# Performance work log

Hardware: AMD Instinct MI355X
Metric: run time of the kernel (lower is better)

## Reference

```python
import jax, jax.numpy as jnp
import numpy as np

VOCAB, D, S, T, B, E, C = 21128, 768, 50, 5, 512, 128, 10


def gcn(x, edges, W, b):
    # GCNConv with self-loops and symmetric normalization. x: [S, D]
    N = x.shape[0]
    loop = jnp.arange(N)
    src = jnp.concatenate([edges[0], loop])
    dst = jnp.concatenate([edges[1], loop])
    deg = jax.ops.segment_sum(jnp.ones_like(src, dtype=x.dtype), dst, num_segments=N)
    dinv = jax.lax.rsqrt(jnp.maximum(deg, 1e-12))
    norm = dinv[src] * dinv[dst]
    h = x @ W  # [S, 10]
    out = jax.ops.segment_sum(h[src] * norm[:, None], dst, num_segments=N)
    return out + b


def mpm(self_f, cross_f, assign, W1, b1, W2, b2):
    # multi-perspective matching, broadcast over leading dims; node dim = -2
    a = assign * self_f
    c = assign * cross_f
    num = jnp.sum(a * c, axis=-1)
    den = jnp.maximum(jnp.linalg.norm(a, axis=-1) * jnp.linalg.norm(c, axis=-1), 1e-8)
    cos = num / den
    bshape = jnp.broadcast_shapes(self_f.shape[:-2], cross_f.shape[:-2])
    sf = jnp.broadcast_to(self_f, bshape + self_f.shape[-2:])
    h = jnp.concatenate([cos[..., None], sf], axis=-1)  # [..., S, 11]
    h = jax.nn.relu(h @ W1 + b1) @ W2 + b2  # [..., S, 20]
    return jnp.max(h, axis=-2)  # [..., 20]


def setup_inputs() -> dict:
    key = jax.random.key(0)
    ks = jax.random.split(key, 20)
    inp = {
        "context_input": jax.random.randint(ks[0], (B, T, S), 0, VOCAB),
        "response_input": jax.random.randint(ks[1], (B, S), 0, VOCAB),
        "context_graph_adjs": jax.random.randint(ks[2], (B, T, 2, E), 0, S),
        "response_graph_adj": jax.random.randint(ks[3], (B, 2, E), 0, S),
        "word_emb": jax.random.normal(ks[4], (VOCAB, D), jnp.float32) * 0.02,
        "conv_W": jax.random.normal(ks[5], (D, C), jnp.float32) * 0.05,
        "conv_b": jnp.zeros((C,), jnp.float32),
        "cross_w": jax.random.uniform(ks[6], (D, C), jnp.float32),
        "attention_coef": jax.random.uniform(ks[7], (S, S), jnp.float32),
        "assign_weight": jax.random.uniform(ks[8], (S, C), jnp.float32),
        "mp_W1": jax.random.normal(ks[9], (C + 1, 20), jnp.float32) * 0.3,
        "mp_b1": jnp.zeros((20,), jnp.float32),
        "mp_W2": jax.random.normal(ks[10], (20, 20), jnp.float32) * 0.2,
        "mp_b2": jnp.zeros((20,), jnp.float32),
        "ffn_W1": jax.random.normal(ks[11], (80, 40), jnp.float32) * 0.1,
        "ffn_b1": jnp.zeros((40,), jnp.float32),
        "ffn_W2": jax.random.normal(ks[12], (40, 1), jnp.float32) * 0.2,
        "ffn_b2": jnp.zeros((1,), jnp.float32),
    }
    return inp


def reference(context_input, response_input, context_graph_adjs, response_graph_adj,
              word_emb, conv_W, conv_b, cross_w, attention_coef, assign_weight,
              mp_W1, mp_b1, mp_W2, mp_b2, ffn_W1, ffn_b1, ffn_W2, ffn_b2):
    ctx = word_emb[context_input]      # [B, T, S, D]
    resp = word_emb[response_input]    # [B, S, D]

    gcn_b = jax.vmap(gcn, in_axes=(0, 0, None, None))
    resp_gcn = gcn_b(resp, response_graph_adj, conv_W, conv_b)                      # [B, S, C]
    ctx_gcn = jax.vmap(gcn_b, in_axes=(0, 0, None, None))(ctx, context_graph_adjs, conv_W, conv_b)  # [B, T, S, C]

    # cross features: utterance cross comes from response, response cross from utterance
    u_cross = jnp.einsum('ps,bsk->bpk', attention_coef, resp @ cross_w)   # [B, S, C]
    r_cross = jnp.einsum('ps,btsk->btpk', attention_coef, ctx @ cross_w)  # [B, T, S, C]

    g_u = mpm(ctx_gcn, u_cross[:, None], assign_weight, mp_W1, mp_b1, mp_W2, mp_b2)       # [B, T, 20]
    g_r = mpm(resp_gcn[:, None], r_cross, assign_weight, mp_W1, mp_b1, mp_W2, mp_b2)      # [B, T, 20]

    feat = jnp.concatenate([g_u, g_r, g_u * g_r, jnp.abs(g_u - g_r)], axis=-1)  # [B, T, 80]
    logits = jax.nn.relu(feat @ ffn_W1 + ffn_b1) @ ffn_W2 + ffn_b2              # [B, T, 1]
    return jax.nn.sigmoid(jnp.sum(logits, axis=1))                              # [B, 1]
```

## Files before the change

kernel.cpp:

```cpp
#include <hip/hip_runtime.h>
#include <math.h>

#define VOCAB 21128
#define DD 768
#define SS 50
#define TT 5
#define BB 512
#define EE 128
#define CC 10
#define V20 (VOCAB * 20)
#define NG 2560
#define NALL 3072

__global__ __launch_bounds__(512) void k_vocab(const float* __restrict__ emb,
                                               const float* __restrict__ Wconv,
                                               const float* __restrict__ Wcross,
                                               float* __restrict__ hvp) {
    __shared__ float tile[8][64][21];
    const int wv = threadIdx.x >> 6, lane = threadIdx.x & 63;
    const int rowbase = blockIdx.x * 64;
    const int rsub = lane >> 2, m = lane & 3;

    const int d0w = blockIdx.y * 384 + __builtin_amdgcn_readfirstlane(wv * 48);

    float4 v[12];
#pragma unroll
    for (int ch = 0; ch < 3; ++ch) {
#pragma unroll
        for (int it = 0; it < 4; ++it) {
            int row = it * 16 + rsub;
            long r = rowbase + row;
            if (r >= VOCAB) r = VOCAB - 1;
            v[ch * 4 + it] = *(const float4*)(emb + r * DD + d0w + ch * 16 + m * 4);
        }
    }

    float acc[20];
#pragma unroll
    for (int c = 0; c < 20; c++) acc[c] = 0.f;

#pragma unroll
    for (int ch = 0; ch < 3; ++ch) {
        const int d0 = d0w + ch * 16;
#pragma unroll
        for (int it = 0; it < 4; ++it) {
            const int row = it * 16 + rsub;
            const float4 w = v[ch * 4 + it];
            tile[wv][row][m * 4 + 0] = w.x;
            tile[wv][row][m * 4 + 1] = w.y;
            tile[wv][row][m * 4 + 2] = w.z;
            tile[wv][row][m * 4 + 3] = w.w;
        }
#pragma unroll
        for (int d = 0; d < 16; ++d) {
            float e = tile[wv][lane][d];
            const float* wc = Wconv + (d0 + d) * 10;
            const float* wx = Wcross + (d0 + d) * 10;
#pragma unroll
            for (int c = 0; c < 10; c++) {
                acc[c] = fmaf(e, wc[c], acc[c]);
                acc[10 + c] = fmaf(e, wx[c], acc[10 + c]);
            }
        }
    }

    __syncthreads();
    float* pp = &tile[0][0][0];
#pragma unroll
    for (int c = 0; c < 20; c++) pp[wv * 1280 + lane * 20 + c] = acc[c];
    __syncthreads();
    float* outp = hvp + (long)blockIdx.y * V20;
    for (int i = threadIdx.x; i < 1280; i += 512) {
        int row = i / 20;
        long r = rowbase + row;
        if (r < VOCAB) {
            float s = 0.f;
#pragma unroll
            for (int w = 0; w < 8; ++w) s += pp[w * 1280 + i];
            outp[r * 20 + (i - row * 20)] = s;
        }
    }
}

__global__ __launch_bounds__(256) void k_gcn(const int* __restrict__ ctok,
                                             const int* __restrict__ cadj,
                                             const int* __restrict__ rtok,
                                             const int* __restrict__ radj,
                                             const float* __restrict__ hvp,
                                             const float* __restrict__ convb,
                                             const float* __restrict__ att,
                                             float* __restrict__ P) {
    __shared__ float attT[SS][51];
    __shared__ float hcv[4][SS][12];
    __shared__ float hcx[4][SS][12];
    __shared__ float aggL[4][SS][11];
    __shared__ int dgS[4][64];
    const int tid = threadIdx.x, wv = tid >> 6, lane = tid & 63;
    const int G = blockIdx.x * 4 + wv;

    for (int i = tid; i < SS * SS; i += 256) { int p = i / SS, s = i - p * SS; attT[s][p] = att[i]; }
    __syncthreads();

    const int* tb;
    const int* ab;
    if (G < NG) { tb = ctok + (long)G * SS; ab = cadj + (long)G * 2 * EE; }
    else        { int b = G - NG; tb = rtok + (long)b * SS; ab = radj + (long)b * 2 * EE; }

    const int e1s = ab[lane], e2s = ab[lane + 64];
    const int e1d = ab[EE + lane], e2d = ab[EE + lane + 64];
    const int myTok = (lane < SS) ? tb[lane] : 0;

    dgS[wv][lane] = 0;
    atomicAdd(&dgS[wv][e1d], 1);
    atomicAdd(&dgS[wv][e2d], 1);

    const float4* hv4 = (const float4*)hvp;
#pragma unroll
    for (int it = 0; it < 4; ++it) {
        const int idx = it * 64 + lane;
        int row = idx / 5;
        const int q = idx - row * 5;
        const int rowc = (row < SS) ? row : (SS - 1);
        const int t = __shfl(myTok, rowc);
        if (idx < SS * 5) {
            const float4 a = hv4[(long)t * 5 + q];
            const float4 b = hv4[(long)(VOCAB * 5) + (long)t * 5 + q];
            const float4 w = make_float4(a.x + b.x, a.y + b.y, a.z + b.z, a.w + b.w);
            if (q == 0)      *(float4*)&hcv[wv][row][0] = w;
            else if (q == 1) *(float4*)&hcv[wv][row][4] = w;
            else if (q == 2) { hcv[wv][row][8] = w.x; hcv[wv][row][9] = w.y;
                               hcx[wv][row][0] = w.z; hcx[wv][row][1] = w.w; }
            else if (q == 3) { *(float2*)&hcx[wv][row][2] = make_float2(w.x, w.y);
                               *(float2*)&hcx[wv][row][4] = make_float2(w.z, w.w); }
            else             { *(float2*)&hcx[wv][row][6] = make_float2(w.x, w.y);
                               *(float2*)&hcx[wv][row][8] = make_float2(w.z, w.w); }
        }
    }

    float dv = 0.f;
    if (lane < SS) dv = rsqrtf((float)(dgS[wv][lane] + 1));

    float* aggW = &aggL[wv][0][0];
    for (int i = lane; i < SS * 11; i += 64) aggW[i] = 0.f;
    const float n1 = __shfl(dv, e1s) * __shfl(dv, e1d);
    const float n2 = __shfl(dv, e2s) * __shfl(dv, e2d);
#pragma unroll
    for (int c = 0; c < CC; c++) atomicAdd(&aggW[e1d * 11 + c], hcv[wv][e1s][c] * n1);
#pragma unroll
    for (int c = 0; c < CC; c++) atomicAdd(&aggW[e2d * 11 + c], hcv[wv][e2s][c] * n2);

    const int p = lane;
    if (p < SS) {
        float gcn[CC], ax[CC];
        const float dp2 = dv * dv;
        const float4 s0 = *(const float4*)&hcv[wv][p][0];
        const float4 s1 = *(const float4*)&hcv[wv][p][4];
        const float s8 = hcv[wv][p][8], s9 = hcv[wv][p][9];
        gcn[0] = aggW[p * 11 + 0] + s0.x * dp2 + convb[0];
        gcn[1] = aggW[p * 11 + 1] + s0.y * dp2 + convb[1];
        gcn[2] = aggW[p * 11 + 2] + s0.z * dp2 + convb[2];
        gcn[3] = aggW[p * 11 + 3] + s0.w * dp2 + convb[3];
        gcn[4] = aggW[p * 11 + 4] + s1.x * dp2 + convb[4];
        gcn[5] = aggW[p * 11 + 5] + s1.y * dp2 + convb[5];
        gcn[6] = aggW[p * 11 + 6] + s1.z * dp2 + convb[6];
        gcn[7] = aggW[p * 11 + 7] + s1.w * dp2 + convb[7];
        gcn[8] = aggW[p * 11 + 8] + s8 * dp2 + convb[8];
        gcn[9] = aggW[p * 11 + 9] + s9 * dp2 + convb[9];
#pragma unroll
        for (int c = 0; c < CC; c++) ax[c] = 0.f;
#pragma unroll 5
        for (int s = 0; s < SS; ++s) {
            const float a = attT[s][p];
            const float4 x0 = *(const float4*)&hcx[wv][s][0];
            const float4 x1 = *(const float4*)&hcx[wv][s][4];
            const float2 x2 = *(const float2*)&hcx[wv][s][8];
            ax[0] = fmaf(a, x0.x, ax[0]); ax[1] = fmaf(a, x0.y, ax[1]);
            ax[2] = fmaf(a, x0.z, ax[2]); ax[3] = fmaf(a, x0.w, ax[3]);
            ax[4] = fmaf(a, x1.x, ax[4]); ax[5] = fmaf(a, x1.y, ax[5]);
            ax[6] = fmaf(a, x1.z, ax[6]); ax[7] = fmaf(a, x1.w, ax[7]);
            ax[8] = fmaf(a, x2.x, ax[8]); ax[9] = fmaf(a, x2.y, ax[9]);
        }
        float4* o4 = (float4*)(P + (long)G * 1000 + p * 20);
        o4[0] = make_float4(gcn[0], gcn[1], gcn[2], gcn[3]);
        o4[1] = make_float4(gcn[4], gcn[5], gcn[6], gcn[7]);
        o4[2] = make_float4(gcn[8], gcn[9], ax[0], ax[1]);
        o4[3] = make_float4(ax[2], ax[3], ax[4], ax[5]);
        o4[4] = make_float4(ax[6], ax[7], ax[8], ax[9]);
    }
}

__global__ __launch_bounds__(256) void k_mpm(const float* __restrict__ P,
                                             const float* __restrict__ assign,
                                             const float* __restrict__ W1, const float* __restrict__ b1,
                                             const float* __restrict__ W2, const float* __restrict__ b2,
                                             float* __restrict__ guG,
                                             float* __restrict__ grG) {
    __shared__ float W2T[20][21];
    __shared__ float asgL[SS][11];
    __shared__ float h1L[4][SS][20];
    const int tid = threadIdx.x, wv = tid >> 6, lane = tid & 63;
    const int wid = blockIdx.x * 4 + wv;
    const int g = wid >> 1, which = wid & 1;
    const int b = g / TT;

    for (int i = tid; i < 400; i += 256) W2T[i % 20][i / 20] = W2[i];
    for (int i = tid; i < SS * CC; i += 256) asgL[i / CC][i % CC] = assign[i];
    __syncthreads();

    const float* Pc = P + (long)g * 1000;
    const float* Pr = P + (long)(NG + b) * 1000;
    const float* selfP = which ? Pr : Pc;
    const float* croP  = which ? Pc : Pr;

    const int p = lane;
    float self[CC], cro[CC];
    if (p < SS) {
        const float4* s4 = (const float4*)(selfP + p * 20);
        const float4 a0 = s4[0], a1 = s4[1], a2 = s4[2];
        self[0] = a0.x; self[1] = a0.y; self[2] = a0.z; self[3] = a0.w;
        self[4] = a1.x; self[5] = a1.y; self[6] = a1.z; self[7] = a1.w;
        self[8] = a2.x; self[9] = a2.y;
        const float4* c4 = (const float4*)(croP + p * 20);
        const float4 b0 = c4[2], b1q = c4[3], b2q = c4[4];
        cro[0] = b0.z; cro[1] = b0.w;
        cro[2] = b1q.x; cro[3] = b1q.y; cro[4] = b1q.z; cro[5] = b1q.w;
        cro[6] = b2q.x; cro[7] = b2q.y; cro[8] = b2q.z; cro[9] = b2q.w;
    }

    const int j = lane % 20;
    const int grp = lane / 20;
    float w2r[20];
#pragma unroll
    for (int k = 0; k < 20; k++) w2r[k] = W2T[j][k];

    if (p < SS) {
        float num = 0.f, na = 0.f, nc2 = 0.f;
#pragma unroll
        for (int c = 0; c < CC; c++) {
            float av = asgL[p][c];
            float a = av * self[c];
            float cx = av * cro[c];
            num = fmaf(a, cx, num);
            na = fmaf(a, a, na);
            nc2 = fmaf(cx, cx, nc2);
        }
        float cosv = num / fmaxf(sqrtf(na) * sqrtf(nc2), 1e-8f);
        float h1[20];
#pragma unroll
        for (int q = 0; q < 20; q++) h1[q] = fmaf(cosv, W1[q], b1[q]);
#pragma unroll
        for (int k = 0; k < CC; k++) {
            float sv = self[k];
#pragma unroll
            for (int q = 0; q < 20; q++) h1[q] = fmaf(sv, W1[(k + 1) * 20 + q], h1[q]);
        }
        float4* hw = (float4*)&h1L[wv][p][0];
        hw[0] = make_float4(fmaxf(h1[0], 0.f), fmaxf(h1[1], 0.f), fmaxf(h1[2], 0.f), fmaxf(h1[3], 0.f));
        hw[1] = make_float4(fmaxf(h1[4], 0.f), fmaxf(h1[5], 0.f), fmaxf(h1[6], 0.f), fmaxf(h1[7], 0.f));
        hw[2] = make_float4(fmaxf(h1[8], 0.f), fmaxf(h1[9], 0.f), fmaxf(h1[10], 0.f), fmaxf(h1[11], 0.f));
        hw[3] = make_float4(fmaxf(h1[12], 0.f), fmaxf(h1[13], 0.f), fmaxf(h1[14], 0.f), fmaxf(h1[15], 0.f));
        hw[4] = make_float4(fmaxf(h1[16], 0.f), fmaxf(h1[17], 0.f), fmaxf(h1[18], 0.f), fmaxf(h1[19], 0.f));
    }

    float part = -1e30f;
    if (grp < 3) {
        const int s0 = grp * 17;
        const int s1 = (grp == 2) ? SS : (s0 + 17);
        for (int s = s0; s < s1; ++s) {
            const float* hr = &h1L[wv][s][0];
            float t = 0.f;
#pragma unroll
            for (int k = 0; k < 20; k++) t = fmaf(hr[k], w2r[k], t);
            part = fmaxf(part, t);
        }
    }
    const float a0 = __shfl(part, j);
    const float a1 = __shfl(part, j + 20);
    const float a2 = __shfl(part, j + 40);
    if (lane < 20) {
        float h2 = fmaxf(fmaxf(a0, a1), a2) + b2[lane];
        (which ? grG : guG)[(long)g * 20 + lane] = h2;
    }
}

__global__ __launch_bounds__(64) void k_final(const float* __restrict__ g_u, const float* __restrict__ g_r,
                                              const float* __restrict__ W1, const float* __restrict__ b1,
                                              const float* __restrict__ W2, const float* __restrict__ b2,
                                              float* __restrict__ out) {
    const int b = blockIdx.x, lane = threadIdx.x;
    float ssum = 0.f;
    for (int t = 0; t < TT; t++) {
        const float* gu = g_u + ((long)b * TT + t) * 20;
        const float* gr = g_r + ((long)b * TT + t) * 20;
        float feat[80];
#pragma unroll
        for (int k = 0; k < 20; k++) {
            float u = gu[k], r = gr[k];
            feat[k] = u;
            feat[20 + k] = r;
            feat[40 + k] = u * r;
            feat[60 + k] = fabsf(u - r);
        }
        if (lane < 40) {
            float hv = b1[lane];
#pragma unroll
            for (int k = 0; k < 80; k++) hv = fmaf(feat[k], W1[k * 40 + lane], hv);
            ssum += fmaxf(hv, 0.f) * W2[lane];
        }
    }
    for (int off = 32; off; off >>= 1) ssum += __shfl_xor(ssum, off);
    if (lane == 0) out[b] = 1.f / (1.f + expf(-(ssum + (float)TT * b2[0])));
}

extern "C" void kernel_launch(void* const* d_in, const int* in_sizes, int n_in,
                              void* d_out, int out_size, void* d_ws, size_t ws_size,
                              hipStream_t stream) {
    (void)in_sizes; (void)n_in; (void)out_size; (void)ws_size;
    const int* ctx_tok = (const int*)d_in[0];
    const int* resp_tok = (const int*)d_in[1];
    const int* ctx_adj = (const int*)d_in[2];
    const int* resp_adj = (const int*)d_in[3];
    const float* emb = (const float*)d_in[4];
    const float* convW = (const float*)d_in[5];
    const float* convb = (const float*)d_in[6];
    const float* crossW = (const float*)d_in[7];
    const float* att = (const float*)d_in[8];
    const float* assign = (const float*)d_in[9];
    const float* mpW1 = (const float*)d_in[10];
    const float* mpb1 = (const float*)d_in[11];
    const float* mpW2 = (const float*)d_in[12];
    const float* mpb2 = (const float*)d_in[13];
    const float* fW1 = (const float*)d_in[14];
    const float* fb1 = (const float*)d_in[15];
    const float* fW2 = (const float*)d_in[16];
    const float* fb2 = (const float*)d_in[17];

    float* ws = (float*)d_ws;
    float* hvp = ws;
    float* P = hvp + 2 * V20;
    float* guG = P + (long)NALL * 1000;
    float* grG = guG + (long)NG * 20;
    float* outf = (float*)d_out;

    hipLaunchKernelGGL(k_vocab, dim3((VOCAB + 63) / 64, 2), dim3(512), 0, stream,
                       emb, convW, crossW, hvp);
    hipLaunchKernelGGL(k_gcn, dim3(NALL / 4), dim3(256), 0, stream,
                       ctx_tok, ctx_adj, resp_tok, resp_adj, hvp, convb, att, P);
    hipLaunchKernelGGL(k_mpm, dim3(NG * 2 / 4), dim3(256), 0, stream,
                       P, assign, mpW1, mpb1, mpW2, mpb2, guG, grG);
    hipLaunchKernelGGL(k_final, dim3(BB), dim3(64), 0, stream,
                       guG, grG, fW1, fb1, fW2, fb2, outf);
}
```

Measured before the change: 79.22 us.

## Redistribute attention matmul across waves and replace mpm reduction with LDS atomicMax

A tiny prep kernel now writes the transposed attention matrix to global memory, with rows padded to 52. This removes the per-block shared-memory transpose and its barrier in k_gcn. The cross-attention product is restructured so each lane owns one (graph, channel) pair and 13 output positions, reading wave-uniform attention rows. In k_mpm, the shared-memory h1 buffer and the strided second-layer max are replaced by per-lane 20x20 matvecs with W2 read from global memory, followed by an order-preserving integer atomicMax in LDS. This trades barriers and shuffles for more per-lane FLOPs, extra LDS atomic contention and one additional kernel launch.

```diff
diff --git a/kernel.cpp b/kernel.cpp
--- a/kernel.cpp
+++ b/kernel.cpp
@@ -12,6 +12,22 @@
 #define NG 2560
 #define NALL 3072
 
+__device__ __forceinline__ unsigned fenc(float f) {
+    unsigned u = __float_as_uint(f);
+    return (u & 0x80000000u) ? ~u : (u | 0x80000000u);
+}
+__device__ __forceinline__ float fdec(unsigned u) {
+    return (u & 0x80000000u) ? __uint_as_float(u & 0x7fffffffu) : __uint_as_float(~u);
+}
+
+__global__ void k_prep(const float* __restrict__ att, float* __restrict__ attT) {
+    int i = blockIdx.x * 64 + threadIdx.x;
+    if (i < SS * SS) {
+        int p = i / SS, s = i - p * SS;
+        attT[s * 52 + p] = att[i];
+    }
+}
+
 __global__ __launch_bounds__(512) void k_vocab(const float* __restrict__ emb,
                                                const float* __restrict__ Wconv,
                                                const float* __restrict__ Wcross,
@@ -88,18 +104,14 @@
                                              const int* __restrict__ radj,
                                              const float* __restrict__ hvp,
                                              const float* __restrict__ convb,
-                                             const float* __restrict__ att,
+                                             const float* __restrict__ attT,
                                              float* __restrict__ P) {
-    __shared__ float attT[SS][51];
+    __shared__ float hcx[4][SS][12];
     __shared__ float hcv[4][SS][12];
-    __shared__ float hcx[4][SS][12];
     __shared__ float aggL[4][SS][11];
     __shared__ int dgS[4][64];
     const int tid = threadIdx.x, wv = tid >> 6, lane = tid & 63;
     const int G = blockIdx.x * 4 + wv;
-
-    for (int i = tid; i < SS * SS; i += 256) { int p = i / SS, s = i - p * SS; attT[s][p] = att[i]; }
-    __syncthreads();
 
     const int* tb;
     const int* ab;
@@ -151,7 +163,7 @@
 
     const int p = lane;
     if (p < SS) {
-        float gcn[CC], ax[CC];
+        float gcn[CC];
         const float dp2 = dv * dv;
         const float4 s0 = *(const float4*)&hcv[wv][p][0];
         const float4 s1 = *(const float4*)&hcv[wv][p][4];
@@ -166,26 +178,32 @@
         gcn[7] = aggW[p * 11 + 7] + s1.w * dp2 + convb[7];
         gcn[8] = aggW[p * 11 + 8] + s8 * dp2 + convb[8];
         gcn[9] = aggW[p * 11 + 9] + s9 * dp2 + convb[9];
-#pragma unroll
-        for (int c = 0; c < CC; c++) ax[c] = 0.f;
-#pragma unroll 5
-        for (int s = 0; s < SS; ++s) {
-            const float a = attT[s][p];
-            const float4 x0 = *(const float4*)&hcx[wv][s][0];
-            const float4 x1 = *(const float4*)&hcx[wv][s][4];
-            const float2 x2 = *(const float2*)&hcx[wv][s][8];
-            ax[0] = fmaf(a, x0.x, ax[0]); ax[1] = fmaf(a, x0.y, ax[1]);
-            ax[2] = fmaf(a, x0.z, ax[2]); ax[3] = fmaf(a, x0.w, ax[3]);
-            ax[4] = fmaf(a, x1.x, ax[4]); ax[5] = fmaf(a, x1.y, ax[5]);
-            ax[6] = fmaf(a, x1.z, ax[6]); ax[7] = fmaf(a, x1.w, ax[7]);
-            ax[8] = fmaf(a, x2.x, ax[8]); ax[9] = fmaf(a, x2.y, ax[9]);
-        }
-        float4* o4 = (float4*)(P + (long)G * 1000 + p * 20);
-        o4[0] = make_float4(gcn[0], gcn[1], gcn[2], gcn[3]);
-        o4[1] = make_float4(gcn[4], gcn[5], gcn[6], gcn[7]);
-        o4[2] = make_float4(gcn[8], gcn[9], ax[0], ax[1]);
-        o4[3] = make_float4(ax[2], ax[3], ax[4], ax[5]);
-        o4[4] = make_float4(ax[6], ax[7], ax[8], ax[9]);
+        float* o = P + (long)G * 1000 + p * 20;
+        *(float4*)(o + 0) = make_float4(gcn[0], gcn[1], gcn[2], gcn[3]);
+        *(float4*)(o + 4) = make_float4(gcn[4], gcn[5], gcn[6], gcn[7]);
+        *(float2*)(o + 8) = make_float2(gcn[8], gcn[9]);
+    }
+    __syncthreads();
+
+    const int l = (lane < 40) ? lane : 39;
+    const int Gl = l / 10, c = l - Gl * 10;
+    const int pbase = __builtin_amdgcn_readfirstlane(wv * 13);
+    float ax[13];
+#pragma unroll
+    for (int pi = 0; pi < 13; ++pi) ax[pi] = 0.f;
+    for (int s = 0; s < SS; ++s) {
+        const float x = hcx[Gl][s][c];
+        const float* ar = attT + s * 52 + pbase;
+#pragma unroll
+        for (int pi = 0; pi < 13; ++pi) ax[pi] = fmaf(ar[pi], x, ax[pi]);
+    }
+    if (lane < 40) {
+        const long Gg = (long)blockIdx.x * 4 + Gl;
+#pragma unroll
+        for (int pi = 0; pi < 13; ++pi) {
+            const int pp = pbase + pi;
+            if (pp < SS) P[Gg * 1000 + pp * 20 + 10 + c] = ax[pi];
+        }
     }
 }
 
@@ -195,15 +213,13 @@
                                              const float* __restrict__ W2, const float* __restrict__ b2,
                                              float* __restrict__ guG,
                                              float* __restrict__ grG) {
-    __shared__ float W2T[20][21];
     __shared__ float asgL[SS][11];
-    __shared__ float h1L[4][SS][20];
+    __shared__ unsigned h2U[4][20];
     const int tid = threadIdx.x, wv = tid >> 6, lane = tid & 63;
     const int wid = blockIdx.x * 4 + wv;
     const int g = wid >> 1, which = wid & 1;
     const int b = g / TT;
 
-    for (int i = tid; i < 400; i += 256) W2T[i % 20][i / 20] = W2[i];
     for (int i = tid; i < SS * CC; i += 256) asgL[i / CC][i % CC] = assign[i];
     __syncthreads();
 
@@ -214,6 +230,8 @@
 
     const int p = lane;
     float self[CC], cro[CC];
+#pragma unroll
+    for (int c = 0; c < CC; c++) { self[c] = 0.f; cro[c] = 0.f; }
     if (p < SS) {
         const float4* s4 = (const float4*)(selfP + p * 20);
         const float4 a0 = s4[0], a1 = s4[1], a2 = s4[2];
@@ -227,58 +245,47 @@
         cro[6] = b2q.x; cro[7] = b2q.y; cro[8] = b2q.z; cro[9] = b2q.w;
     }
 
-    const int j = lane % 20;
-    const int grp = lane / 20;
-    float w2r[20];
-#pragma unroll
-    for (int k = 0; k < 20; k++) w2r[k] = W2T[j][k];
-
+    float num = 0.f, na = 0.f, nc2 = 0.f;
+#pragma unroll
+    for (int c = 0; c < CC; c++) {
+        float av = asgL[(p < SS) ? p : 0][c];
+        float a = av * self[c];
+        float cx = av * cro[c];
+        num = fmaf(a, cx, num);
+        na = fmaf(a, a, na);
+        nc2 = fmaf(cx, cx, nc2);
+    }
+    float cosv = num / fmaxf(sqrtf(na) * sqrtf(nc2), 1e-8f);
+    float h1[20];
+#pragma unroll
+    for (int q = 0; q < 20; q++) h1[q] = fmaf(cosv, W1[q], b1[q]);
+#pragma unroll
+    for (int k = 0; k < CC; k++) {
+        float sv = self[k];
+#pragma unroll
+        for (int q = 0; q < 20; q++) h1[q] = fmaf(sv, W1[(k + 1) * 20 + q], h1[q]);
+    }
+#pragma unroll
+    for (int q = 0; q < 20; q++) h1[q] = fmaxf(h1[q], 0.f);
+
+    if (lane < 20) h2U[wv][lane] = 0u;
+
+    float v[20];
+#pragma unroll
+    for (int j = 0; j < 20; j++) v[j] = 0.f;
+#pragma unroll 4
+    for (int k = 0; k < 20; k++) {
+        const float hk = h1[k];
+        const float* wr = W2 + k * 20;
+#pragma unroll
+        for (int j = 0; j < 20; j++) v[j] = fmaf(hk, wr[j], v[j]);
+    }
     if (p < SS) {
-        float num = 0.f, na = 0.f, nc2 = 0.f;
-#pragma unroll
-        for (int c = 0; c < CC; c++) {
-            float av = asgL[p][c];
-            float a = av * self[c];
-            float cx = av * cro[c];
-            num = fmaf(a, cx, num);
-            na = fmaf(a, a, na);
-            nc2 = fmaf(cx, cx, nc2);
-        }
-        float cosv = num / fmaxf(sqrtf(na) * sqrtf(nc2), 1e-8f);
-        float h1[20];
-#pragma unroll
-        for (int q = 0; q < 20; q++) h1[q] = fmaf(cosv, W1[q], b1[q]);
-#pragma unroll
-        for (int k = 0; k < CC; k++) {
-            float sv = self[k];
-#pragma unroll
-            for (int q = 0; q < 20; q++) h1[q] = fmaf(sv, W1[(k + 1) * 20 + q], h1[q]);
-        }
-        float4* hw = (float4*)&h1L[wv][p][0];
-        hw[0] = make_float4(fmaxf(h1[0], 0.f), fmaxf(h1[1], 0.f), fmaxf(h1[2], 0.f), fmaxf(h1[3], 0.f));
-        hw[1] = make_float4(fmaxf(h1[4], 0.f), fmaxf(h1[5], 0.f), fmaxf(h1[6], 0.f), fmaxf(h1[7], 0.f));
-        hw[2] = make_float4(fmaxf(h1[8], 0.f), fmaxf(h1[9], 0.f), fmaxf(h1[10], 0.f), fmaxf(h1[11], 0.f));
-        hw[3] = make_float4(fmaxf(h1[12], 0.f), fmaxf(h1[13], 0.f), fmaxf(h1[14], 0.f), fmaxf(h1[15], 0.f));
-        hw[4] = make_float4(fmaxf(h1[16], 0.f), fmaxf(h1[17], 0.f), fmaxf(h1[18], 0.f), fmaxf(h1[19], 0.f));
-    }
-
-    float part = -1e30f;
-    if (grp < 3) {
-        const int s0 = grp * 17;
-        const int s1 = (grp == 2) ? SS : (s0 + 17);
-        for (int s = s0; s < s1; ++s) {
-            const float* hr = &h1L[wv][s][0];
-            float t = 0.f;
-#pragma unroll
-            for (int k = 0; k < 20; k++) t = fmaf(hr[k], w2r[k], t);
-            part = fmaxf(part, t);
-        }
-    }
-    const float a0 = __shfl(part, j);
-    const float a1 = __shfl(part, j + 20);
-    const float a2 = __shfl(part, j + 40);
+#pragma unroll
+        for (int j = 0; j < 20; j++) atomicMax(&h2U[wv][j], fenc(v[j]));
+    }
     if (lane < 20) {
-        float h2 = fmaxf(fmaxf(a0, a1), a2) + b2[lane];
+        float h2 = fdec(h2U[wv][lane]) + b2[lane];
         (which ? grG : guG)[(long)g * 20 + lane] = h2;
     }
 }
@@ -338,14 +345,16 @@
     float* ws = (float*)d_ws;
     float* hvp = ws;
     float* P = hvp + 2 * V20;
-    float* guG = P + (long)NALL * 1000;
+    float* attT = P + (long)NALL * 1000;
+    float* guG = attT + 2600;
     float* grG = guG + (long)NG * 20;
     float* outf = (float*)d_out;
 
+    hipLaunchKernelGGL(k_prep, dim3(40), dim3(64), 0, stream, att, attT);
     hipLaunchKernelGGL(k_vocab, dim3((VOCAB + 63) / 64, 2), dim3(512), 0, stream,
                        emb, convW, crossW, hvp);
     hipLaunchKernelGGL(k_gcn, dim3(NALL / 4), dim3(256), 0, stream,
-                       ctx_tok, ctx_adj, resp_tok, resp_adj, hvp, convb, att, P);
+                       ctx_tok, ctx_adj, resp_tok, resp_adj, hvp, convb, attT, P);
     hipLaunchKernelGGL(k_mpm, dim3(NG * 2 / 4), dim3(256), 0, stream,
                        P, assign, mpW1, mpb1, mpW2, mpb2, guG, grG);
     hipLaunchKernelGGL(k_final, dim3(BB), dim3(64), 0, stream,
```

Measured after the change: 93.68 us. 18.3% more time.
